# Performance work log

Measured on AMD Instinct MI355X. Metric: run time of the kernel, lower is better.

The kernel has to match this reference:

```python
import jax, jax.numpy as jnp
import numpy as np

DIM = 2048
BATCH = 16384
EPS = 1e-12


def setup_inputs() -> dict:
    key = jax.random.key(0)
    ks = jax.random.split(key, 12)
    d = DIM
    inp = {
        "h_final": jax.random.normal(ks[0], (BATCH, d), dtype=jnp.float32),
        "v_claim": jax.random.normal(ks[1], (BATCH, d), dtype=jnp.float32),
        "v_doc": jax.random.normal(ks[2], (BATCH, d), dtype=jnp.float32),
        # feature_extractor: Linear(d+3, d) -> ReLU -> Linear(d, d//2) -> ReLU
        "W1": jax.random.normal(ks[3], (d + 3, d), dtype=jnp.float32) / np.sqrt(d + 3),
        "b1": jnp.zeros((d,), dtype=jnp.float32),
        "W2": jax.random.normal(ks[4], (d, d // 2), dtype=jnp.float32) / np.sqrt(d),
        "b2": jnp.zeros((d // 2,), dtype=jnp.float32),
        # retrieval head: Linear(d//2, 1) -> Sigmoid
        "Wr": jax.random.normal(ks[5], (d // 2, 1), dtype=jnp.float32) / np.sqrt(d // 2),
        "br": jnp.zeros((1,), dtype=jnp.float32),
    }
    return inp


def reference(h_final, v_claim, v_doc, W1, b1, W2, b2, Wr, br):
    # L2-normalize claim/doc vectors (F.normalize with eps clamp)
    cn = v_claim / jnp.maximum(jnp.linalg.norm(v_claim, axis=-1, keepdims=True), EPS)
    dn = v_doc / jnp.maximum(jnp.linalg.norm(v_doc, axis=-1, keepdims=True), EPS)
    # alignment = cosine similarity (vectors already unit norm) -> [B, 1]
    align = jnp.sum(cn * dn, axis=-1, keepdims=True)
    # divergence = 1 - alignment; tension = divergence^2
    div = 1.0 - align
    tens = div * div
    features = jnp.concatenate([h_final, align, div, tens], axis=-1)  # [B, d+3]
    h = jax.nn.relu(features @ W1 + b1)
    shared = jax.nn.relu(h @ W2 + b2)  # [B, d//2]
    out = jax.nn.sigmoid(shared @ Wr + br)  # [B, 1] (task='retrieval')
    return out
```

## Files before the change

kernel.cpp:

```cpp
#include <hip/hip_runtime.h>
#include <hip/hip_bf16.h>
#include <stdint.h>

#define BATCH 16384
#define DIM   2048
#define DIM2  1024

typedef __attribute__((ext_vector_type(8))) short short8;
typedef __attribute__((ext_vector_type(4))) float f32x4;

__device__ __forceinline__ ushort f2bf(float f) {
  uint32_t u = __float_as_uint(f);
  u += 0x7fffu + ((u >> 16) & 1u);
  return (ushort)(u >> 16);
}
__device__ __forceinline__ float bf2f(ushort h) {
  return __uint_as_float(((uint32_t)h) << 16);
}

__device__ __forceinline__ void gload_lds16(const void* g, void* l) {
  __builtin_amdgcn_global_load_lds(
      (__attribute__((address_space(1))) void*)g,
      (__attribute__((address_space(3))) void*)l,
      16, 0, 0);
}

__device__ __forceinline__ f32x4 MFMA(short8 a, short8 b, f32x4 c) {
  return __builtin_amdgcn_mfma_f32_16x16x32_bf16(a, b, c, 0, 0, 0);
}

__global__ void __launch_bounds__(256) prep_kernel(const float* __restrict__ vc,
                                                   const float* __restrict__ vd,
                                                   float* __restrict__ feats) {
  int row = blockIdx.x;
  int t = threadIdx.x;
  const float4* c = (const float4*)(vc + (size_t)row * DIM);
  const float4* d = (const float4*)(vd + (size_t)row * DIM);
  float dot = 0.f, c2 = 0.f, d2 = 0.f;
#pragma unroll
  for (int p = 0; p < 2; ++p) {
    float4 a = c[t * 2 + p];
    float4 b = d[t * 2 + p];
    dot += a.x * b.x + a.y * b.y + a.z * b.z + a.w * b.w;
    c2  += a.x * a.x + a.y * a.y + a.z * a.z + a.w * a.w;
    d2  += b.x * b.x + b.y * b.y + b.z * b.z + b.w * b.w;
  }
#pragma unroll
  for (int off = 32; off >= 1; off >>= 1) {
    dot += __shfl_down(dot, off, 64);
    c2  += __shfl_down(c2, off, 64);
    d2  += __shfl_down(d2, off, 64);
  }
  __shared__ float red[3][4];
  int l = t & 63, w = t >> 6;
  if (l == 0) { red[0][w] = dot; red[1][w] = c2; red[2][w] = d2; }
  __syncthreads();
  if (t == 0) {
    float D  = red[0][0] + red[0][1] + red[0][2] + red[0][3];
    float C2 = red[1][0] + red[1][1] + red[1][2] + red[1][3];
    float D2 = red[2][0] + red[2][1] + red[2][2] + red[2][3];
    float nc = fmaxf(sqrtf(C2), 1e-12f);
    float nd = fmaxf(sqrtf(D2), 1e-12f);
    float align = D / (nc * nd);
    float dv = 1.f - align;
    feats[row] = align;
    feats[BATCH + row] = dv;
    feats[2 * BATCH + row] = dv * dv;
  }
}

__global__ void __launch_bounds__(256) cvt_kernel(const float* __restrict__ in,
                                                  ushort* __restrict__ out) {
  size_t i = (size_t)blockIdx.x * 256 + threadIdx.x;
  const float4* p = (const float4*)in;
  float4 f0 = p[2 * i], f1 = p[2 * i + 1];
  uint4 u;
  u.x = (uint32_t)f2bf(f0.x) | ((uint32_t)f2bf(f0.y) << 16);
  u.y = (uint32_t)f2bf(f0.z) | ((uint32_t)f2bf(f0.w) << 16);
  u.z = (uint32_t)f2bf(f1.x) | ((uint32_t)f2bf(f1.y) << 16);
  u.w = (uint32_t)f2bf(f1.z) | ((uint32_t)f2bf(f1.w) << 16);
  ((uint4*)out)[i] = u;
}

__global__ void __launch_bounds__(256) transW(const float* __restrict__ W,
                                              ushort* __restrict__ WT,
                                              int K, int N) {
  __shared__ float tile[32][33];
  int t = threadIdx.x;
  int tx = t & 31, ty = t >> 5;
  int c0 = blockIdx.x * 32, r0 = blockIdx.y * 32;
#pragma unroll
  for (int p = 0; p < 4; ++p)
    tile[ty + p * 8][tx] = W[(size_t)(r0 + ty + p * 8) * N + c0 + tx];
  __syncthreads();
#pragma unroll
  for (int p = 0; p < 4; ++p) {
    int rr = ty + p * 8;
    WT[(size_t)(c0 + rr) * K + r0 + tx] = f2bf(tile[tx][rr]);
  }
}

template <int MODE, int N>
__global__ void __launch_bounds__(512, 1) gemm256(const ushort* __restrict__ A,
                                                  const ushort* __restrict__ BT,
                                                  ushort* __restrict__ C,
                                                  const float* __restrict__ feats,
                                                  const float* __restrict__ wex,
                                                  const float* __restrict__ bias) {
  constexpr int K = 2048;
  constexpr int NT = K / 64;
  __shared__ __align__(16) char lds[131072];
  const int tid = threadIdx.x;
  const int l = tid & 63, w = tid >> 6;
  const int wr = w >> 2, wc = w & 3;
  const int l4 = l & 15, lhi = l >> 4;

  constexpr int GX = N / 256;
  const int bid = blockIdx.x;
  const int tx = bid % GX, ty = bid / GX;
  const size_t rowBase = (size_t)ty * 256;
  const int colBase = tx * 256;

  const int swz = (l4 & 7) << 4;
  const int aoffBase = l4 * 128 + ((wr * 64 + lhi * 16) ^ swz);
  const int boffBase = ((wc & 1) * 64 + l4) * 128 + (((wc >> 1) * 64 + lhi * 16) ^ swz);

  const char* pAs[2];
  const char* pBs[2];
#pragma unroll
  for (int c = 0; c < 2; ++c) {
    int o = c * 8192 + tid * 16;
    int r = o >> 7, b0 = o & 127;
    int bsw = b0 ^ ((r & 7) << 4);
    int hb = bsw >> 6, cb = bsw & 63;
    pAs[c] = (const char*)A + (rowBase + hb * 128 + r) * (2 * K) + cb;
    pBs[c] = (const char*)BT + ((size_t)colBase + hb * 128 + r) * (2 * K) + cb;
  }
  const int ldso0 = w * 1024;
  const int ldso1 = 8192 + w * 1024;

#define STAGE(srcT, destPar, M, kh)                                          \
  do {                                                                       \
    char* dst_ = lds + (destPar) * 65536 + (kh) * 32768 + (M) * 16384;       \
    const char* s0_ = ((M) ? pBs[0] : pAs[0]) + (srcT) * 128 + (kh) * 64;    \
    const char* s1_ = ((M) ? pBs[1] : pAs[1]) + (srcT) * 128 + (kh) * 64;    \
    gload_lds16(s0_, dst_ + ldso0);                                          \
    gload_lds16(s1_, dst_ + ldso1);                                          \
    asm volatile("" ::: "memory");                                           \
  } while (0)

#define LOADA(q, d, kh)                                                      \
  do {                                                                       \
    const char* sb_ = lds + (d) * 65536 + (kh) * 32768;                      \
    aq[0] = *(const short8*)(sb_ + ((q) * 4 + 0) * 2048 + aoffBase);         \
    aq[1] = *(const short8*)(sb_ + ((q) * 4 + 1) * 2048 + aoffBase);         \
    aq[2] = *(const short8*)(sb_ + ((q) * 4 + 2) * 2048 + aoffBase);         \
    aq[3] = *(const short8*)(sb_ + ((q) * 4 + 3) * 2048 + aoffBase);         \
  } while (0)

#define LOADB(d, kh)                                                         \
  do {                                                                       \
    const char* sb_ = lds + (d) * 65536 + (kh) * 32768 + 16384;              \
    bq[0] = *(const short8*)(sb_ + 0 * 2048 + boffBase);                     \
    bq[1] = *(const short8*)(sb_ + 1 * 2048 + boffBase);                     \
    bq[2] = *(const short8*)(sb_ + 2 * 2048 + boffBase);                     \
    bq[3] = *(const short8*)(sb_ + 3 * 2048 + boffBase);                     \
  } while (0)

#define MF(q)                                                                \
  do {                                                                       \
    _Pragma("unroll") for (int j_ = 0; j_ < 4; ++j_)                         \
        _Pragma("unroll") for (int n_ = 0; n_ < 4; ++n_)                     \
            acc[(q) * 4 + j_][n_] = MFMA(aq[j_], bq[n_], acc[(q) * 4 + j_][n_]); \
  } while (0)

#define BAR()     __builtin_amdgcn_s_barrier()
#define LGKM0()   asm volatile("s_waitcnt lgkmcnt(0)" ::: "memory")
#define VM8()     asm volatile("s_waitcnt vmcnt(8)" ::: "memory")
#define PRIO(x)   __builtin_amdgcn_s_setprio(x)

  f32x4 acc[8][4];
#pragma unroll
  for (int i = 0; i < 8; ++i)
#pragma unroll
    for (int j = 0; j < 4; ++j) acc[i][j] = (f32x4){0.f, 0.f, 0.f, 0.f};

  STAGE(0, 0, 0, 0);
  STAGE(0, 0, 1, 0);
  STAGE(0, 0, 0, 1);
  STAGE(0, 0, 1, 1);
  STAGE(1, 1, 0, 0);
  STAGE(1, 1, 1, 0);
  VM8();
  BAR();

  for (int I = 0; I < NT / 2; ++I) {
    const int o = 2 * I + 1;
    const int e2 = (2 * I + 2 < NT) ? 2 * I + 2 : 0;
    const int o2 = (2 * I + 3 < NT) ? 2 * I + 3 : 0;
    short8 aq[4], bq[4];
    LOADB(0, 0);
    LOADA(0, 0, 0);
    STAGE(o, 1, 0, 1);
    BAR(); LGKM0();
    PRIO(1); MF(0); PRIO(0);
    BAR();
    LOADA(1, 0, 0);
    STAGE(o, 1, 1, 1);
    BAR(); LGKM0();
    PRIO(1); MF(1); PRIO(0);
    VM8();
    BAR();
    LOADB(0, 1);
    LOADA(0, 0, 1);
    STAGE(e2, 0, 0, 0);
    BAR(); LGKM0();
    PRIO(1); MF(0); PRIO(0);
    BAR();
    LOADA(1, 0, 1);
    STAGE(e2, 0, 1, 0);
    BAR(); LGKM0();
    PRIO(1); MF(1); PRIO(0);
    VM8();
    BAR();
    LOADB(1, 0);
    LOADA(0, 1, 0);
    STAGE(e2, 0, 0, 1);
    BAR(); LGKM0();
    PRIO(1); MF(0); PRIO(0);
    BAR();
    LOADA(1, 1, 0);
    STAGE(e2, 0, 1, 1);
    BAR(); LGKM0();
    PRIO(1); MF(1); PRIO(0);
    VM8();
    BAR();
    LOADB(1, 1);
    LOADA(0, 1, 1);
    STAGE(o2, 1, 0, 0);
    BAR(); LGKM0();
    PRIO(1); MF(0); PRIO(0);
    BAR();
    LOADA(1, 1, 1);
    STAGE(o2, 1, 1, 0);
    BAR(); LGKM0();
    PRIO(1); MF(1); PRIO(0);
    VM8();
    BAR();
  }
  asm volatile("s_waitcnt vmcnt(0)" ::: "memory");

  int ccv[4];
  float bb[4], wa[4], wb2[4], wc3[4];
#pragma unroll
  for (int n = 0; n < 4; ++n) {
    int cc = colBase + wc * 64 + n * 16 + l4;
    ccv[n] = cc;
    bb[n] = bias[cc];
    if (MODE == 1) {
      wa[n] = wex[cc]; wb2[n] = wex[2048 + cc]; wc3[n] = wex[4096 + cc];
    } else {
      wa[n] = 0.f; wb2[n] = 0.f; wc3[n] = 0.f;
    }
  }
  const int lhi4 = lhi * 4;
#pragma unroll
  for (int m = 0; m < 8; ++m) {
#pragma unroll
    for (int r = 0; r < 4; ++r) {
      size_t rr = rowBase + wr * 128 + m * 16 + lhi4 + r;
      float f1 = 0.f, f2 = 0.f, f3 = 0.f;
      if (MODE == 1) {
        f1 = feats[rr]; f2 = feats[BATCH + rr]; f3 = feats[2 * BATCH + rr];
      }
#pragma unroll
      for (int n = 0; n < 4; ++n) {
        float v = acc[m][n][r] + bb[n];
        if (MODE == 1) v += f1 * wa[n] + f2 * wb2[n] + f3 * wc3[n];
        v = fmaxf(v, 0.f);
        C[rr * N + ccv[n]] = f2bf(v);
      }
    }
  }
#undef STAGE
#undef LOADA
#undef LOADB
#undef MF
#undef BAR
#undef LGKM0
#undef VM8
#undef PRIO
}

__global__ void __launch_bounds__(256) head_kernel(const ushort* __restrict__ S,
                                                   const float* __restrict__ Wr,
                                                   const float* __restrict__ br,
                                                   float* __restrict__ out) {
  int row = blockIdx.x * 4 + (threadIdx.x >> 6);
  int l = threadIdx.x & 63;
  const ushort* s = S + (size_t)row * DIM2 + l * 16;
  const float4* wp = (const float4*)(Wr + l * 16);
  uint4 u0 = *(const uint4*)s;
  uint4 u1 = *(const uint4*)(s + 8);
  float4 w0 = wp[0], w1 = wp[1], w2 = wp[2], w3 = wp[3];
  float sum = 0.f;
  sum += bf2f((ushort)(u0.x & 0xffff)) * w0.x + bf2f((ushort)(u0.x >> 16)) * w0.y;
  sum += bf2f((ushort)(u0.y & 0xffff)) * w0.z + bf2f((ushort)(u0.y >> 16)) * w0.w;
  sum += bf2f((ushort)(u0.z & 0xffff)) * w1.x + bf2f((ushort)(u0.z >> 16)) * w1.y;
  sum += bf2f((ushort)(u0.w & 0xffff)) * w1.z + bf2f((ushort)(u0.w >> 16)) * w1.w;
  sum += bf2f((ushort)(u1.x & 0xffff)) * w2.x + bf2f((ushort)(u1.x >> 16)) * w2.y;
  sum += bf2f((ushort)(u1.y & 0xffff)) * w2.z + bf2f((ushort)(u1.y >> 16)) * w2.w;
  sum += bf2f((ushort)(u1.z & 0xffff)) * w3.x + bf2f((ushort)(u1.z >> 16)) * w3.y;
  sum += bf2f((ushort)(u1.w & 0xffff)) * w3.z + bf2f((ushort)(u1.w >> 16)) * w3.w;
#pragma unroll
  for (int off = 32; off >= 1; off >>= 1) sum += __shfl_down(sum, off, 64);
  if (l == 0) out[row] = 1.f / (1.f + expf(-(sum + br[0])));
}

extern "C" void kernel_launch(void* const* d_in, const int* in_sizes, int n_in,
                              void* d_out, int out_size, void* d_ws, size_t ws_size,
                              hipStream_t stream) {
  const float* h_final = (const float*)d_in[0];
  const float* v_claim = (const float*)d_in[1];
  const float* v_doc   = (const float*)d_in[2];
  const float* W1      = (const float*)d_in[3];
  const float* b1      = (const float*)d_in[4];
  const float* W2      = (const float*)d_in[5];
  const float* b2      = (const float*)d_in[6];
  const float* Wr      = (const float*)d_in[7];
  const float* br      = (const float*)d_in[8];
  float* out = (float*)d_out;

  char* ws = (char*)d_ws;
  ushort* Abf   = (ushort*)ws;
  ushort* Hbf   = (ushort*)(ws + 67108864);
  ushort* W1T   = (ushort*)(ws + 134217728);
  ushort* W2T   = (ushort*)(ws + 142606336);
  float*  feats = (float*)(ws + 146800640);
  ushort* Sbf   = Abf;

  prep_kernel<<<BATCH, 256, 0, stream>>>(v_claim, v_doc, feats);
  cvt_kernel<<<(BATCH * DIM / 8) / 256, 256, 0, stream>>>(h_final, Abf);
  transW<<<dim3(DIM / 32, DIM / 32), 256, 0, stream>>>(W1, W1T, DIM, DIM);
  transW<<<dim3(DIM2 / 32, DIM / 32), 256, 0, stream>>>(W2, W2T, DIM, DIM2);

  gemm256<1, DIM><<<(DIM / 256) * (BATCH / 256), 512, 0, stream>>>(
      Abf, W1T, Hbf, feats, W1 + (size_t)2048 * 2048, b1);
  gemm256<2, DIM2><<<(DIM2 / 256) * (BATCH / 256), 512, 0, stream>>>(
      Hbf, W2T, Sbf, nullptr, nullptr, b2);

  head_kernel<<<BATCH / 4, 256, 0, stream>>>(Sbf, Wr, br, out);
}
```

Before: 289.7 us.

## Fuse h_final bf16 conversion into prep kernel and drop explicit lgkmcnt waits

The h_final fp32-to-bf16 conversion is merged into the row-wise alignment prep kernel, removing one launch and letting each block read its row of all three inputs together. In the GEMM main loop, the explicit s_waitcnt lgkmcnt(0) after each barrier becomes a compiler memory fence, so the compiler inserts only the waits each LDS-to-register load needs before the MFMAs. This is meant to let LDS reads overlap with MFMA issue. It relies on the compiler's automatic waitcnt handling staying correct around the asynchronous global_load_lds writes and the barriers.

```diff
diff --git a/kernel.cpp b/kernel.cpp
--- a/kernel.cpp
+++ b/kernel.cpp
@@ -29,9 +29,11 @@
   return __builtin_amdgcn_mfma_f32_16x16x32_bf16(a, b, c, 0, 0, 0);
 }
 
-__global__ void __launch_bounds__(256) prep_kernel(const float* __restrict__ vc,
-                                                   const float* __restrict__ vd,
-                                                   float* __restrict__ feats) {
+__global__ void __launch_bounds__(256) prep_fused(const float* __restrict__ vc,
+                                                  const float* __restrict__ vd,
+                                                  const float* __restrict__ h,
+                                                  ushort* __restrict__ hbf,
+                                                  float* __restrict__ feats) {
   int row = blockIdx.x;
   int t = threadIdx.x;
   const float4* c = (const float4*)(vc + (size_t)row * DIM);
@@ -44,6 +46,16 @@
     dot += a.x * b.x + a.y * b.y + a.z * b.z + a.w * b.w;
     c2  += a.x * a.x + a.y * a.y + a.z * a.z + a.w * a.w;
     d2  += b.x * b.x + b.y * b.y + b.z * b.z + b.w * b.w;
+  }
+  {
+    const float4* hp = (const float4*)(h + (size_t)row * DIM);
+    float4 f0 = hp[t * 2], f1 = hp[t * 2 + 1];
+    uint4 u;
+    u.x = (uint32_t)f2bf(f0.x) | ((uint32_t)f2bf(f0.y) << 16);
+    u.y = (uint32_t)f2bf(f0.z) | ((uint32_t)f2bf(f0.w) << 16);
+    u.z = (uint32_t)f2bf(f1.x) | ((uint32_t)f2bf(f1.y) << 16);
+    u.w = (uint32_t)f2bf(f1.z) | ((uint32_t)f2bf(f1.w) << 16);
+    ((uint4*)hbf)[(size_t)row * 256 + t] = u;
   }
 #pragma unroll
   for (int off = 32; off >= 1; off >>= 1) {
@@ -69,19 +81,6 @@
   }
 }
 
-__global__ void __launch_bounds__(256) cvt_kernel(const float* __restrict__ in,
-                                                  ushort* __restrict__ out) {
-  size_t i = (size_t)blockIdx.x * 256 + threadIdx.x;
-  const float4* p = (const float4*)in;
-  float4 f0 = p[2 * i], f1 = p[2 * i + 1];
-  uint4 u;
-  u.x = (uint32_t)f2bf(f0.x) | ((uint32_t)f2bf(f0.y) << 16);
-  u.y = (uint32_t)f2bf(f0.z) | ((uint32_t)f2bf(f0.w) << 16);
-  u.z = (uint32_t)f2bf(f1.x) | ((uint32_t)f2bf(f1.y) << 16);
-  u.w = (uint32_t)f2bf(f1.z) | ((uint32_t)f2bf(f1.w) << 16);
-  ((uint4*)out)[i] = u;
-}
-
 __global__ void __launch_bounds__(256) transW(const float* __restrict__ W,
                                               ushort* __restrict__ WT,
                                               int K, int N) {
@@ -175,7 +174,7 @@
   } while (0)
 
 #define BAR()     __builtin_amdgcn_s_barrier()
-#define LGKM0()   asm volatile("s_waitcnt lgkmcnt(0)" ::: "memory")
+#define MEMF()    asm volatile("" ::: "memory")
 #define VM8()     asm volatile("s_waitcnt vmcnt(8)" ::: "memory")
 #define PRIO(x)   __builtin_amdgcn_s_setprio(x)
 
@@ -193,6 +192,7 @@
   STAGE(1, 1, 1, 0);
   VM8();
   BAR();
+  MEMF();
 
   for (int I = 0; I < NT / 2; ++I) {
     const int o = 2 * I + 1;
@@ -202,51 +202,51 @@
     LOADB(0, 0);
     LOADA(0, 0, 0);
     STAGE(o, 1, 0, 1);
-    BAR(); LGKM0();
+    BAR(); MEMF();
     PRIO(1); MF(0); PRIO(0);
-    BAR();
+    BAR(); MEMF();
     LOADA(1, 0, 0);
     STAGE(o, 1, 1, 1);
-    BAR(); LGKM0();
+    BAR(); MEMF();
     PRIO(1); MF(1); PRIO(0);
     VM8();
-    BAR();
+    BAR(); MEMF();
     LOADB(0, 1);
     LOADA(0, 0, 1);
     STAGE(e2, 0, 0, 0);
-    BAR(); LGKM0();
+    BAR(); MEMF();
     PRIO(1); MF(0); PRIO(0);
-    BAR();
+    BAR(); MEMF();
     LOADA(1, 0, 1);
     STAGE(e2, 0, 1, 0);
-    BAR(); LGKM0();
+    BAR(); MEMF();
     PRIO(1); MF(1); PRIO(0);
     VM8();
-    BAR();
+    BAR(); MEMF();
     LOADB(1, 0);
     LOADA(0, 1, 0);
     STAGE(e2, 0, 0, 1);
-    BAR(); LGKM0();
+    BAR(); MEMF();
     PRIO(1); MF(0); PRIO(0);
-    BAR();
+    BAR(); MEMF();
     LOADA(1, 1, 0);
     STAGE(e2, 0, 1, 1);
-    BAR(); LGKM0();
+    BAR(); MEMF();
     PRIO(1); MF(1); PRIO(0);
     VM8();
-    BAR();
+    BAR(); MEMF();
     LOADB(1, 1);
     LOADA(0, 1, 1);
     STAGE(o2, 1, 0, 0);
-    BAR(); LGKM0();
+    BAR(); MEMF();
     PRIO(1); MF(0); PRIO(0);
-    BAR();
+    BAR(); MEMF();
     LOADA(1, 1, 1);
     STAGE(o2, 1, 1, 0);
-    BAR(); LGKM0();
+    BAR(); MEMF();
     PRIO(1); MF(1); PRIO(0);
     VM8();
-    BAR();
+    BAR(); MEMF();
   }
   asm volatile("s_waitcnt vmcnt(0)" ::: "memory");
 
@@ -287,7 +287,7 @@
 #undef LOADB
 #undef MF
 #undef BAR
-#undef LGKM0
+#undef MEMF
 #undef VM8
 #undef PRIO
 }
@@ -339,8 +339,7 @@
   float*  feats = (float*)(ws + 146800640);
   ushort* Sbf   = Abf;
 
-  prep_kernel<<<BATCH, 256, 0, stream>>>(v_claim, v_doc, feats);
-  cvt_kernel<<<(BATCH * DIM / 8) / 256, 256, 0, stream>>>(h_final, Abf);
+  prep_fused<<<BATCH, 256, 0, stream>>>(v_claim, v_doc, h_final, Abf, feats);
   transW<<<dim3(DIM / 32, DIM / 32), 256, 0, stream>>>(W1, W1T, DIM, DIM);
   transW<<<dim3(DIM2 / 32, DIM / 32), 256, 0, stream>>>(W2, W2T, DIM, DIM2);
 
```

Measured after the change: 294.2 us. About the same (+1.5%).
